# Optimization experiments

Hardware: AMD Instinct MI355X
Metric: run time of the kernel (lower is better)

The kernel has to match this reference:

```python
import jax, jax.numpy as jnp
import numpy as np
from jax import lax

B, T, N, F_IN, F_OUT, K = 16, 12, 2048, 32, 64, 3
TK = 3  # temporal kernel


def setup_inputs() -> dict:
    key = jax.random.key(0)
    ks = jax.random.split(key, 10)
    s = lambda fan: 1.0 / np.sqrt(fan)
    return {
        "x": jax.random.normal(ks[0], (B, T, N, F_IN), jnp.float32),
        "cheb": jax.random.normal(ks[1], (K, N, N), jnp.float32) * s(N),
        "wq_t": jax.random.normal(ks[2], (F_IN, 1), jnp.float32) * s(F_IN),
        "wk_t": jax.random.normal(ks[3], (F_IN, 1), jnp.float32) * s(F_IN),
        "wq_s": jax.random.normal(ks[4], (F_IN, 1), jnp.float32) * s(F_IN),
        "wk_s": jax.random.normal(ks[5], (F_IN, 1), jnp.float32) * s(F_IN),
        "theta": jax.random.normal(ks[6], (K, F_IN, F_OUT), jnp.float32) * s(F_IN),
        "tconv_w": jax.random.normal(ks[7], (F_OUT, F_OUT, TK, 1), jnp.float32) * s(F_OUT * TK),
        "tconv_b": jnp.zeros((F_OUT,), jnp.float32),
        "rconv_w": jax.random.normal(ks[8], (F_OUT, F_IN), jnp.float32) * s(F_IN),
        "rconv_b": jnp.zeros((F_OUT,), jnp.float32),
        "ln_g": jnp.ones((F_OUT,), jnp.float32),
        "ln_b": jnp.zeros((F_OUT,), jnp.float32),
    }


def reference(x, cheb, wq_t, wk_t, wq_s, wk_s, theta, tconv_w, tconv_b,
              rconv_w, rconv_b, ln_g, ln_b):
    b, t, n, f = x.shape
    # --- temporal attention: (B,T,T) over time, scaled by sqrt(N)
    qt = jnp.einsum('btnf,fo->btn', x, wq_t)  # (B,T,N)
    kt = jnp.einsum('btnf,fo->btn', x, wk_t)
    ta = jax.nn.softmax(jnp.einsum('btn,bsn->bts', qt, kt) / np.sqrt(n), axis=-1)
    x_ta = jnp.einsum('bts,bsnf->btnf', ta, x)
    # --- spatial attention: (B,N,N), scaled by sqrt(history_len)
    qs = jnp.einsum('btnf,fo->btn', x_ta, wq_s)
    ks_ = jnp.einsum('btnf,fo->btn', x_ta, wk_s)
    sa = jax.nn.softmax(jnp.einsum('btn,btm->bnm', qs, ks_) / np.sqrt(t), axis=-1)
    # --- Chebyshev graph conv with attention-weighted polynomials
    out = jnp.zeros((b, t, n, theta.shape[-1]), x.dtype)
    for kk in range(cheb.shape[0]):  # small fixed K
        tka = cheb[kk][None, :, :] * sa              # (B,N,N)
        rhs = jnp.einsum('bij,btjf->btif', tka, x_ta)  # (B,T,N,F_in)
        out = out + jnp.einsum('btif,fo->btio', rhs, theta[kk])
    x_gc = jax.nn.relu(out)  # (B,T,N,O)
    # --- temporal conv over T (kernel (3,1), pad (1,0)), NCHW with H=T, W=N
    xc = x_gc.transpose(0, 3, 1, 2)
    pad = TK // 2
    x_tc = lax.conv_general_dilated(
        xc, tconv_w, window_strides=(1, 1), padding=((pad, pad), (0, 0)),
        dimension_numbers=('NCHW', 'OIHW', 'NCHW'))
    x_tc = x_tc + tconv_b[None, :, None, None]
    # --- 1x1 residual conv on original x
    res = jnp.einsum('btnf,of->botn', x, rconv_w) + rconv_b[None, :, None, None]
    y = jax.nn.relu(x_tc + res).transpose(0, 2, 3, 1)  # (B,T,N,O)
    # --- layer norm over channels
    mu = jnp.mean(y, axis=-1, keepdims=True)
    var = jnp.mean((y - mu) ** 2, axis=-1, keepdims=True)
    return (y - mu) * lax.rsqrt(var + 1e-5) * ln_g + ln_b
```

## Files before the change

kernel.cpp:

```cpp
#include <hip/hip_runtime.h>
#include <hip/hip_bf16.h>
#include <math.h>

#define BB 16
#define TT 12
#define NN 2048
#define FIN 32
#define FOUT 64
#define KCH 3

typedef __attribute__((ext_vector_type(8))) short vbf16x8;
typedef __attribute__((ext_vector_type(4))) float vf32x4;

__device__ __forceinline__ float ldf(const void* p, size_t i, int mf) {
    if (mf) return ((const float*)p)[i];
    return __bfloat162float(((const __hip_bfloat16*)p)[i]);
}

__device__ __forceinline__ void load8d(const void* p, size_t i, int mf, float* o) {
    if (mf) {
        const float* fp = (const float*)p + i;
        float4 a = *(const float4*)fp;
        float4 b = *(const float4*)(fp + 4);
        o[0] = a.x; o[1] = a.y; o[2] = a.z; o[3] = a.w;
        o[4] = b.x; o[5] = b.y; o[6] = b.z; o[7] = b.w;
    } else {
        uint4 u = *(const uint4*)((const __hip_bfloat16*)p + i);
        const __hip_bfloat16* h = (const __hip_bfloat16*)&u;
#pragma unroll
        for (int j = 0; j < 8; ++j) o[j] = __bfloat162float(h[j]);
    }
}

__device__ __forceinline__ vbf16x8 pack8(const float* v) {
    union { vbf16x8 f; __hip_bfloat16 h[8]; } u;
#pragma unroll
    for (int j = 0; j < 8; ++j) u.h[j] = __float2bfloat16(v[j]);
    return u.f;
}

__global__ __launch_bounds__(256) void k_detect(const void* __restrict__ x, int* __restrict__ flag) {
    __shared__ int cnt[256];
    const unsigned short* h = (const unsigned short*)x;
    int bad = 0;
    for (int i = threadIdx.x; i < 4096; i += 256) {
        int e = (h[i] >> 7) & 0xFF;
        if (e < 110 || e > 133) bad++;
    }
    cnt[threadIdx.x] = bad;
    __syncthreads();
    for (int s = 128; s > 0; s >>= 1) {
        if ((int)threadIdx.x < s) cnt[threadIdx.x] += cnt[threadIdx.x + s];
        __syncthreads();
    }
    if (threadIdx.x == 0) flag[0] = (cnt[0] > 614) ? 1 : 0;
}

__global__ __launch_bounds__(256) void k_emergency(__hip_bfloat16* out, size_t n) {
    size_t i = (size_t)blockIdx.x * 256 + threadIdx.x;
    if (i < n) out[i] = __float2bfloat16(55555.f);
}

__global__ __launch_bounds__(256) void k_cvt_cheb(
    const void* __restrict__ cheb, const int* __restrict__ flag,
    __hip_bfloat16* __restrict__ chebBF) {
    int mf = flag[0];
    size_t i = ((size_t)blockIdx.x * 256 + threadIdx.x) * 8;
    float v[8];
    load8d(cheb, i, mf, v);
    union { uint4 u; __hip_bfloat16 h[8]; } pv;
#pragma unroll
    for (int j = 0; j < 8; ++j) pv.h[j] = __float2bfloat16(v[j]);
    *reinterpret_cast<uint4*>(&chebBF[i]) = pv.u;
}

__global__ __launch_bounds__(256) void k_prep(
    const void* __restrict__ theta, const void* __restrict__ tconv_w,
    const void* __restrict__ tconv_b, const void* __restrict__ rconv_w,
    const void* __restrict__ rconv_b, const int* __restrict__ flag,
    __hip_bfloat16* __restrict__ Tt, __hip_bfloat16* __restrict__ Wt, float* __restrict__ biasC) {
    int mf = flag[0];
    int tid = blockIdx.x * 256 + threadIdx.x;
    if (tid < 64 * 96) {
        int o = tid / 96, kf = tid % 96;
        Tt[tid] = __float2bfloat16(ldf(theta, (size_t)kf * 64 + o, mf));
    }
    if (tid < 64 * 224) {
        int o = tid / 224, c = tid % 224;
        float v;
        if (c < 192) {
            int dt = c / 64, i = c % 64;
            v = ldf(tconv_w, ((size_t)o * 64 + i) * 3 + dt, mf);
        } else {
            v = ldf(rconv_w, (size_t)o * 32 + (c - 192), mf);
        }
        Wt[tid] = __float2bfloat16(v);
    }
    if (tid < 64) biasC[tid] = ldf(tconv_b, tid, mf) + ldf(rconv_b, tid, mf);
}

__global__ __launch_bounds__(256) void k_qtkt(
    const void* __restrict__ x, const void* __restrict__ wq,
    const void* __restrict__ wk, const int* __restrict__ flag,
    float* __restrict__ qt, float* __restrict__ kt) {
    int mf = flag[0];
    __shared__ float swq[32], swk[32];
    if (threadIdx.x < 32) swq[threadIdx.x] = ldf(wq, threadIdx.x, mf);
    else if (threadIdx.x < 64) swk[threadIdx.x - 32] = ldf(wk, threadIdx.x - 32, mf);
    __syncthreads();
    size_t idx = (size_t)blockIdx.x * 256 + threadIdx.x;
    float q = 0.f, k = 0.f;
#pragma unroll
    for (int c = 0; c < 4; ++c) {
        float v[8];
        load8d(x, idx * FIN + c * 8, mf, v);
#pragma unroll
        for (int j = 0; j < 8; ++j) { q += v[j] * swq[c * 8 + j]; k += v[j] * swk[c * 8 + j]; }
    }
    qt[idx] = q;
    kt[idx] = k;
}

__global__ __launch_bounds__(256) void k_tattn(
    const float* __restrict__ qt, const float* __restrict__ kt, float* __restrict__ ta) {
    int b = blockIdx.x / TT, t = blockIdx.x % TT;
    const float* q = qt + ((size_t)b * TT + t) * NN;
    float part[TT];
#pragma unroll
    for (int s = 0; s < TT; ++s) part[s] = 0.f;
    for (int n = threadIdx.x; n < NN; n += 256) {
        float qv = q[n];
#pragma unroll
        for (int s = 0; s < TT; ++s) part[s] += qv * kt[((size_t)b * TT + s) * NN + n];
    }
    __shared__ float red[TT][4];
    __shared__ float sc[TT];
    int lane = threadIdx.x & 63, wid = threadIdx.x >> 6;
#pragma unroll
    for (int s = 0; s < TT; ++s) {
        float v = part[s];
#pragma unroll
        for (int m = 32; m >= 1; m >>= 1) v += __shfl_xor(v, m);
        if (lane == 0) red[s][wid] = v;
    }
    __syncthreads();
    if (threadIdx.x < TT)
        sc[threadIdx.x] = (red[threadIdx.x][0] + red[threadIdx.x][1] + red[threadIdx.x][2] +
                           red[threadIdx.x][3]) * 0.02209708691207961f;
    __syncthreads();
    if (threadIdx.x == 0) {
        float m = sc[0];
#pragma unroll
        for (int s = 1; s < TT; ++s) m = fmaxf(m, sc[s]);
        float e[TT], sum = 0.f;
#pragma unroll
        for (int s = 0; s < TT; ++s) { e[s] = __expf(sc[s] - m); sum += e[s]; }
        float inv = 1.f / sum;
#pragma unroll
        for (int s = 0; s < TT; ++s) ta[((size_t)b * TT + t) * TT + s] = e[s] * inv;
    }
}

__global__ __launch_bounds__(256) void k_xta(
    const void* __restrict__ x, const float* __restrict__ ta,
    const void* __restrict__ wqs, const void* __restrict__ wks, const int* __restrict__ flag,
    __hip_bfloat16* __restrict__ xT, float* __restrict__ qs, float* __restrict__ ks, int b0) {
    int mf = flag[0];
    int gid = blockIdx.x * 256 + threadIdx.x;
    int fg = gid & 3;
    int n = (gid >> 2) & (NN - 1);
    int bl = gid >> 13;
    int b = b0 + bl;
    __shared__ float sta[TT * TT];
    __shared__ float swq[32], swk[32];
    if (threadIdx.x < 144) sta[threadIdx.x] = ta[(size_t)b * 144 + threadIdx.x];
    else if (threadIdx.x >= 160 && threadIdx.x < 192) swq[threadIdx.x - 160] = ldf(wqs, threadIdx.x - 160, mf);
    else if (threadIdx.x >= 192 && threadIdx.x < 224) swk[threadIdx.x - 192] = ldf(wks, threadIdx.x - 192, mf);
    __syncthreads();

    float acc[TT][8];
#pragma unroll
    for (int t = 0; t < TT; ++t)
#pragma unroll
        for (int j = 0; j < 8; ++j) acc[t][j] = 0.f;

    for (int s = 0; s < TT; ++s) {
        float xv[8];
        load8d(x, (((size_t)(b * TT + s) * NN) + n) * FIN + fg * 8, mf, xv);
#pragma unroll
        for (int t = 0; t < TT; ++t) {
            float w = sta[t * TT + s];
#pragma unroll
            for (int j = 0; j < 8; ++j) acc[t][j] += w * xv[j];
        }
    }
    size_t xbase = (size_t)bl * 384 * NN;
#pragma unroll
    for (int t = 0; t < TT; ++t)
#pragma unroll
        for (int j = 0; j < 8; ++j)
            xT[xbase + (size_t)(t * 32 + fg * 8 + j) * NN + n] = __float2bfloat16(acc[t][j]);
#pragma unroll
    for (int t = 0; t < TT; ++t) {
        float pq = 0.f, pk = 0.f;
#pragma unroll
        for (int j = 0; j < 8; ++j) {
            pq += acc[t][j] * swq[fg * 8 + j];
            pk += acc[t][j] * swk[fg * 8 + j];
        }
        pq += __shfl_xor(pq, 1); pq += __shfl_xor(pq, 2);
        pk += __shfl_xor(pk, 1); pk += __shfl_xor(pk, 2);
        if (fg == 0) {
            qs[((size_t)b * NN + n) * TT + t] = pq;
            ks[((size_t)b * NN + n) * TT + t] = pk;
        }
    }
}

__global__ __launch_bounds__(256) void k_sattn(
    const float* __restrict__ qs, const float* __restrict__ ks,
    __hip_bfloat16* __restrict__ sa, int b0) {
    int bl = blockIdx.x >> 8;
    int b = b0 + bl;
    int i0 = (blockIdx.x & 255) * 8;
    __shared__ float qrow[8][TT];
    __shared__ float rbuf[4];
    if (threadIdx.x < 96) qrow[threadIdx.x / TT][threadIdx.x % TT] =
        qs[((size_t)b * NN + i0) * TT + threadIdx.x];
    __syncthreads();
    const float scale = 0.28867513459481287f;
    float sc[8][8];
#pragma unroll
    for (int c = 0; c < 8; ++c) {
        int j = threadIdx.x + (c << 8);
        const float* kr = ks + ((size_t)b * NN + j) * TT;
        float kv[TT];
        *(float4*)&kv[0] = *(const float4*)&kr[0];
        *(float4*)&kv[4] = *(const float4*)&kr[4];
        *(float4*)&kv[8] = *(const float4*)&kr[8];
#pragma unroll
        for (int r = 0; r < 8; ++r) {
            float d = 0.f;
#pragma unroll
            for (int t = 0; t < TT; ++t) d += qrow[r][t] * kv[t];
            sc[r][c] = d * scale;
        }
    }
    int lane = threadIdx.x & 63, wid = threadIdx.x >> 6;
#pragma unroll
    for (int r = 0; r < 8; ++r) {
        float v = -1e30f;
#pragma unroll
        for (int c = 0; c < 8; ++c) v = fmaxf(v, sc[r][c]);
#pragma unroll
        for (int m = 32; m >= 1; m >>= 1) v = fmaxf(v, __shfl_xor(v, m));
        if (lane == 0) rbuf[wid] = v;
        __syncthreads();
        float bmax = fmaxf(fmaxf(rbuf[0], rbuf[1]), fmaxf(rbuf[2], rbuf[3]));
        __syncthreads();
        float lsum = 0.f;
#pragma unroll
        for (int c = 0; c < 8; ++c) { float e = __expf(sc[r][c] - bmax); sc[r][c] = e; lsum += e; }
        v = lsum;
#pragma unroll
        for (int m = 32; m >= 1; m >>= 1) v += __shfl_xor(v, m);
        if (lane == 0) rbuf[wid] = v;
        __syncthreads();
        float inv = 1.f / (rbuf[0] + rbuf[1] + rbuf[2] + rbuf[3]);
        __syncthreads();
        size_t base = ((size_t)bl * NN + i0 + r) * NN + threadIdx.x;
#pragma unroll
        for (int c = 0; c < 8; ++c) sa[base + (c << 8)] = __float2bfloat16(sc[r][c] * inv);
    }
}

__global__ __launch_bounds__(256, 2) void k_gemm_cheb(
    const __hip_bfloat16* __restrict__ chebBF, const __hip_bfloat16* __restrict__ sa,
    const __hip_bfloat16* __restrict__ xT, __hip_bfloat16* __restrict__ rhs) {
    int it = blockIdx.x;
    int bz = blockIdx.y;
    int bl = bz / 3, kk = bz % 3;

    __shared__ __hip_bfloat16 As[2][64][40];

    int tid = threadIdx.x;
    int wid = tid >> 6, lane = tid & 63;
    int wn = wid * 96;
    int lr = lane & 15, kq = (lane >> 4) * 8;

    const size_t i0 = (size_t)it * 64;
    const __hip_bfloat16* chebK = chebBF + (size_t)kk * NN * NN;
    const __hip_bfloat16* saB = sa + (size_t)bl * NN * NN;
    const __hip_bfloat16* xTB = xT + (size_t)bl * 384 * NN;

    int srow = tid >> 2;
    int scol = (tid & 3) * 8;

    const __hip_bfloat16* cptr = &chebK[(i0 + srow) * NN + scol];
    const __hip_bfloat16* sptr = &saB[(i0 + srow) * NN + scol];
    const __hip_bfloat16* bptr0 = &xTB[(size_t)(wn + lr) * NN + kq];

    vf32x4 acc[4][6];
    vf32x4 z4 = {0.f, 0.f, 0.f, 0.f};
#pragma unroll
    for (int mi = 0; mi < 4; ++mi)
#pragma unroll
        for (int ni = 0; ni < 6; ++ni) acc[mi][ni] = z4;

    uint4 cu = *reinterpret_cast<const uint4*>(cptr);
    uint4 su = *reinterpret_cast<const uint4*>(sptr);
    vbf16x8 bcur[6];
#pragma unroll
    for (int ni = 0; ni < 6; ++ni)
        bcur[ni] = *reinterpret_cast<const vbf16x8*>(bptr0 + (size_t)(ni * 16) * NN);

    for (int step = 0; step < 64; ++step) {
        int p = step & 1;
        {
            const __hip_bfloat16* ch = (const __hip_bfloat16*)&cu;
            const __hip_bfloat16* sh = (const __hip_bfloat16*)&su;
            union { uint4 u; __hip_bfloat16 h8[8]; } pv;
#pragma unroll
            for (int j = 0; j < 8; ++j)
                pv.h8[j] = __float2bfloat16(__bfloat162float(ch[j]) * __bfloat162float(sh[j]));
            *reinterpret_cast<uint4*>(&As[p][srow][scol]) = pv.u;
        }

        __syncthreads();

        vbf16x8 a[4];
#pragma unroll
        for (int mi = 0; mi < 4; ++mi)
            a[mi] = *reinterpret_cast<const vbf16x8*>(&As[p][mi * 16 + lr][kq]);

        int joff = (step < 63) ? (step + 1) * 32 : step * 32;
        cu = *reinterpret_cast<const uint4*>(cptr + joff);
        su = *reinterpret_cast<const uint4*>(sptr + joff);
        vbf16x8 bnxt[6];
#pragma unroll
        for (int ni = 0; ni < 6; ++ni)
            bnxt[ni] = *reinterpret_cast<const vbf16x8*>(bptr0 + (size_t)(ni * 16) * NN + joff);

#pragma unroll
        for (int ni = 0; ni < 6; ++ni)
#pragma unroll
            for (int mi = 0; mi < 4; ++mi)
                acc[mi][ni] = __builtin_amdgcn_mfma_f32_16x16x32_bf16(a[mi], bcur[ni], acc[mi][ni], 0, 0, 0);

#pragma unroll
        for (int ni = 0; ni < 6; ++ni) bcur[ni] = bnxt[ni];
    }
#pragma unroll
    for (int mi = 0; mi < 4; ++mi)
#pragma unroll
        for (int ni = 0; ni < 6; ++ni)
#pragma unroll
            for (int g = 0; g < 4; ++g) {
                int row = mi * 16 + ((lane >> 4) << 2) + g;
                int col = wn + ni * 16 + lr;
                size_t i = i0 + row;
                int t = col >> 5, f = col & 31;
                rhs[(((size_t)bl * NN + i) * TT + t) * 96 + kk * 32 + f] =
                    __float2bfloat16(acc[mi][ni][g]);
            }
}

__global__ __launch_bounds__(256) void k_theta(
    const __hip_bfloat16* __restrict__ rhs, const __hip_bfloat16* __restrict__ Tt,
    __hip_bfloat16* __restrict__ G) {
    __shared__ __hip_bfloat16 Ts[64][104];
    int tid = threadIdx.x;
    int srow = tid >> 2, scol = (tid & 3) * 8;
#pragma unroll
    for (int c0 = 0; c0 < 96; c0 += 32)
        *reinterpret_cast<uint4*>(&Ts[srow][c0 + scol]) =
            *reinterpret_cast<const uint4*>(&Tt[(size_t)srow * 96 + c0 + scol]);
    __syncthreads();
    int wid = tid >> 6, lane = tid & 63;
    int lr = lane & 15, kq = (lane >> 4) * 8;
    size_t r0 = (size_t)blockIdx.x * 128 + wid * 32;
    vf32x4 acc[2][4];
    vf32x4 z4 = {0.f, 0.f, 0.f, 0.f};
#pragma unroll
    for (int mi = 0; mi < 2; ++mi)
#pragma unroll
        for (int ni = 0; ni < 4; ++ni) acc[mi][ni] = z4;
#pragma unroll
    for (int s = 0; s < 3; ++s) {
        vbf16x8 a[2], bf[4];
#pragma unroll
        for (int mi = 0; mi < 2; ++mi)
            a[mi] = *reinterpret_cast<const vbf16x8*>(&rhs[(r0 + mi * 16 + lr) * 96 + s * 32 + kq]);
#pragma unroll
        for (int ni = 0; ni < 4; ++ni)
            bf[ni] = *reinterpret_cast<const vbf16x8*>(&Ts[ni * 16 + lr][s * 32 + kq]);
#pragma unroll
        for (int mi = 0; mi < 2; ++mi)
#pragma unroll
            for (int ni = 0; ni < 4; ++ni)
                acc[mi][ni] = __builtin_amdgcn_mfma_f32_16x16x32_bf16(a[mi], bf[ni], acc[mi][ni], 0, 0, 0);
    }
#pragma unroll
    for (int mi = 0; mi < 2; ++mi)
#pragma unroll
        for (int ni = 0; ni < 4; ++ni)
#pragma unroll
            for (int g = 0; g < 4; ++g) {
                size_t r = r0 + mi * 16 + ((lane >> 4) << 2) + g;
                int col = ni * 16 + (lane & 15);
                int t = (int)(r % TT);
                size_t bn = r / TT;
                int n = (int)(bn & (NN - 1));
                int bl = (int)(bn >> 11);
                float v = fmaxf(acc[mi][ni][g], 0.f);
                G[(((size_t)bl * TT + t) * NN + n) * 64 + col] = __float2bfloat16(v);
            }
}

__global__ __launch_bounds__(256) void k_final(
    const __hip_bfloat16* __restrict__ G, const void* __restrict__ x,
    const __hip_bfloat16* __restrict__ Wt, const float* __restrict__ biasC,
    const void* __restrict__ ln_g, const void* __restrict__ ln_b,
    const int* __restrict__ flag, void* __restrict__ outv, int b0) {
    int mf = flag[0];
    int n0 = blockIdx.x * 128;
    int t = blockIdx.y;
    int bl = blockIdx.z;
    int b = b0 + bl;
    __shared__ __hip_bfloat16 Ws[64][232];
    __shared__ float sg[64], sb[64], sbias[64];
    int tid = threadIdx.x;
    int srow = tid >> 2, scol = (tid & 3) * 8;
#pragma unroll
    for (int c0 = 0; c0 < 224; c0 += 32)
        *reinterpret_cast<uint4*>(&Ws[srow][c0 + scol]) =
            *reinterpret_cast<const uint4*>(&Wt[(size_t)srow * 224 + c0 + scol]);
    if (tid < 64) {
        sg[tid] = ldf(ln_g, tid, mf);
        sb[tid] = ldf(ln_b, tid, mf);
        sbias[tid] = biasC[tid];
    }
    __syncthreads();
    int wid = tid >> 6, lane = tid & 63;
    int lr = lane & 15, kq = (lane >> 4) * 8;
    int rw = n0 + wid * 32;
    vf32x4 acc[2][4];
    vf32x4 z4 = {0.f, 0.f, 0.f, 0.f};
#pragma unroll
    for (int mi = 0; mi < 2; ++mi)
#pragma unroll
        for (int ni = 0; ni < 4; ++ni) acc[mi][ni] = z4;

    vbf16x8 zfrag = {0, 0, 0, 0, 0, 0, 0, 0};
#pragma unroll
    for (int s = 0; s < 7; ++s) {
        int kb = s * 32;
        vbf16x8 a[2], bf[4];
#pragma unroll
        for (int ni = 0; ni < 4; ++ni)
            bf[ni] = *reinterpret_cast<const vbf16x8*>(&Ws[ni * 16 + lr][kb + kq]);
        if (s < 6) {
            int dt = s >> 1;
            int t2 = t + dt - 1;
            int off = (s & 1) * 32 + kq;
            if (t2 >= 0 && t2 < TT) {
#pragma unroll
                for (int mi = 0; mi < 2; ++mi)
                    a[mi] = *reinterpret_cast<const vbf16x8*>(
                        &G[(((size_t)bl * TT + t2) * NN + rw + mi * 16 + lr) * 64 + off]);
            } else {
                a[0] = zfrag; a[1] = zfrag;
            }
        } else {
#pragma unroll
            for (int mi = 0; mi < 2; ++mi) {
                float xv[8];
                load8d(x, (((size_t)b * TT + t) * NN + rw + mi * 16 + lr) * FIN + kq, mf, xv);
                a[mi] = pack8(xv);
            }
        }
#pragma unroll
        for (int mi = 0; mi < 2; ++mi)
#pragma unroll
            for (int ni = 0; ni < 4; ++ni)
                acc[mi][ni] = __builtin_amdgcn_mfma_f32_16x16x32_bf16(a[mi], bf[ni], acc[mi][ni], 0, 0, 0);
    }
    float vals[2][4][4];
#pragma unroll
    for (int mi = 0; mi < 2; ++mi)
#pragma unroll
        for (int ni = 0; ni < 4; ++ni) {
            int col = ni * 16 + lr;
#pragma unroll
            for (int g = 0; g < 4; ++g)
                vals[mi][ni][g] = fmaxf(acc[mi][ni][g] + sbias[col], 0.f);
        }
#pragma unroll
    for (int mi = 0; mi < 2; ++mi)
#pragma unroll
        for (int g = 0; g < 4; ++g) {
            float s1 = 0.f, s2 = 0.f;
#pragma unroll
            for (int ni = 0; ni < 4; ++ni) { float v = vals[mi][ni][g]; s1 += v; s2 += v * v; }
            s1 += __shfl_xor(s1, 1); s2 += __shfl_xor(s2, 1);
            s1 += __shfl_xor(s1, 2); s2 += __shfl_xor(s2, 2);
            s1 += __shfl_xor(s1, 4); s2 += __shfl_xor(s2, 4);
            s1 += __shfl_xor(s1, 8); s2 += __shfl_xor(s2, 8);
            float mean = s1 * (1.f / 64.f);
            float var = fmaxf(s2 * (1.f / 64.f) - mean * mean, 0.f);
            float rstd = rsqrtf(var + 1e-5f);
            int row = wid * 32 + mi * 16 + ((lane >> 4) << 2) + g;
#pragma unroll
            for (int ni = 0; ni < 4; ++ni) {
                int col = ni * 16 + lr;
                float y = (vals[mi][ni][g] - mean) * rstd * sg[col] + sb[col];
                size_t oi = (((size_t)b * TT + t) * NN + n0 + row) * 64 + col;
                if (mf) ((float*)outv)[oi] = y;
                else ((__hip_bfloat16*)outv)[oi] = __float2bfloat16(y);
            }
        }
}

extern "C" void kernel_launch(void* const* d_in, const int* in_sizes, int n_in,
                              void* d_out, int out_size, void* d_ws, size_t ws_size,
                              hipStream_t stream) {
    const void* x      = d_in[0];
    const void* cheb   = d_in[1];
    const void* wq_t   = d_in[2];
    const void* wk_t   = d_in[3];
    const void* wq_s   = d_in[4];
    const void* wk_s   = d_in[5];
    const void* theta  = d_in[6];
    const void* tconvw = d_in[7];
    const void* tconvb = d_in[8];
    const void* rconvw = d_in[9];
    const void* rconvb = d_in[10];
    const void* ln_g   = d_in[11];
    const void* ln_b   = d_in[12];

    const size_t sflag = 256;
    const size_t sqt   = (size_t)BB * TT * NN * 4;
    const size_t sta   = 16384;
    const size_t sTt   = 64 * 96 * 2;
    const size_t sWt   = 64 * 224 * 2;
    const size_t sbias = 256;
    const size_t scheb = (size_t)KCH * NN * NN * 2;
    const size_t fixed = sflag + 2 * sqt + sta + sTt + sWt + sbias + scheb;
    const size_t pxT  = (size_t)384 * NN * 2;
    const size_t psa  = (size_t)NN * NN * 2;
    const size_t prhs = (size_t)NN * TT * 96 * 2;
    const size_t perb = pxT + psa + prhs;

    int chk = 0;
    for (int c = 16; c >= 1; c >>= 1)
        if (fixed + (size_t)c * perb <= ws_size) { chk = c; break; }

    if (chk == 0) {
        k_emergency<<<(out_size + 255) / 256, 256, 0, stream>>>(
            (__hip_bfloat16*)d_out, (size_t)out_size);
        return;
    }

    char* ws = (char*)d_ws;
    size_t off = 0;
    int*   flag = (int*)(ws + off);             off += sflag;
    float* qt   = (float*)(ws + off);           off += sqt;
    float* kt   = (float*)(ws + off);           off += sqt;
    float* ta   = (float*)(ws + off);           off += sta;
    __hip_bfloat16* Tt = (__hip_bfloat16*)(ws + off);  off += sTt;
    __hip_bfloat16* Wt = (__hip_bfloat16*)(ws + off);  off += sWt;
    float* biasC = (float*)(ws + off);          off += sbias;
    __hip_bfloat16* chebBF = (__hip_bfloat16*)(ws + off); off += scheb;
    __hip_bfloat16* xTc  = (__hip_bfloat16*)(ws + off); off += (size_t)chk * pxT;
    __hip_bfloat16* saC  = (__hip_bfloat16*)(ws + off); off += (size_t)chk * psa;
    __hip_bfloat16* rhsC = (__hip_bfloat16*)(ws + off); off += (size_t)chk * prhs;
    float* qs = qt;
    float* ks = kt;
    __hip_bfloat16* Gc = saC;

    k_detect<<<1, 256, 0, stream>>>(x, flag);
    k_cvt_cheb<<<(KCH * NN * NN) / 2048, 256, 0, stream>>>(cheb, flag, chebBF);
    k_prep<<<56, 256, 0, stream>>>(theta, tconvw, tconvb, rconvw, rconvb, flag, Tt, Wt, biasC);
    k_qtkt<<<(BB * TT * NN) / 256, 256, 0, stream>>>(x, wq_t, wk_t, flag, qt, kt);
    k_tattn<<<BB * TT, 256, 0, stream>>>(qt, kt, ta);
    for (int b0 = 0; b0 < BB; b0 += chk) {
        k_xta<<<(chk * NN * 4) / 256, 256, 0, stream>>>(x, ta, wq_s, wk_s, flag, xTc, qs, ks, b0);
        k_sattn<<<chk * (NN / 8), 256, 0, stream>>>(qs, ks, saC, b0);
        k_gemm_cheb<<<dim3(32, chk * KCH), 256, 0, stream>>>(chebBF, saC, xTc, rhsC);
        k_theta<<<(chk * NN * TT) / 128, 256, 0, stream>>>(rhsC, Tt, Gc);
        k_final<<<dim3(NN / 128, TT, chk), 256, 0, stream>>>(Gc, x, Wt, biasC, ln_g, ln_b, flag, d_out, b0);
    }
}
```

Measured before the change: 691.2 us.

## Drop LDS staging in cheb GEMM, load A fragments directly with register double-buffering

The Chebyshev-attention GEMM no longer builds the cheb*sa product in shared memory behind a per-step barrier. Each wave now loads its own A fragments from global memory, multiplies them in registers, and double-buffers both A and B loads across two k-steps. The M tile shrinks from 64 to 32 rows and the grid doubles to match. This removes __syncthreads and the LDS round trip. In exchange, every wave re-reads the same A rows (four times the cheb/sa global traffic per block) and B is reused over fewer rows, so more xT traffic overall.

```diff
diff --git a/kernel.cpp b/kernel.cpp
--- a/kernel.cpp
+++ b/kernel.cpp
@@ -36,6 +36,16 @@
     union { vbf16x8 f; __hip_bfloat16 h[8]; } u;
 #pragma unroll
     for (int j = 0; j < 8; ++j) u.h[j] = __float2bfloat16(v[j]);
+    return u.f;
+}
+
+__device__ __forceinline__ vbf16x8 mulpack8(uint4 c, uint4 s) {
+    const __hip_bfloat16* ch = (const __hip_bfloat16*)&c;
+    const __hip_bfloat16* sh = (const __hip_bfloat16*)&s;
+    union { vbf16x8 f; __hip_bfloat16 h[8]; } u;
+#pragma unroll
+    for (int j = 0; j < 8; ++j)
+        u.h[j] = __float2bfloat16(__bfloat162float(ch[j]) * __bfloat162float(sh[j]));
     return u.f;
 }
 
@@ -281,77 +291,64 @@
     int bz = blockIdx.y;
     int bl = bz / 3, kk = bz % 3;
 
-    __shared__ __hip_bfloat16 As[2][64][40];
-
     int tid = threadIdx.x;
     int wid = tid >> 6, lane = tid & 63;
     int wn = wid * 96;
     int lr = lane & 15, kq = (lane >> 4) * 8;
 
-    const size_t i0 = (size_t)it * 64;
-    const __hip_bfloat16* chebK = chebBF + (size_t)kk * NN * NN;
-    const __hip_bfloat16* saB = sa + (size_t)bl * NN * NN;
-    const __hip_bfloat16* xTB = xT + (size_t)bl * 384 * NN;
-
-    int srow = tid >> 2;
-    int scol = (tid & 3) * 8;
-
-    const __hip_bfloat16* cptr = &chebK[(i0 + srow) * NN + scol];
-    const __hip_bfloat16* sptr = &saB[(i0 + srow) * NN + scol];
-    const __hip_bfloat16* bptr0 = &xTB[(size_t)(wn + lr) * NN + kq];
-
-    vf32x4 acc[4][6];
+    const size_t i0 = (size_t)it * 32;
+    const __hip_bfloat16* cA = chebBF + (size_t)kk * NN * NN + (i0 + lr) * NN + kq;
+    const __hip_bfloat16* sA = sa + (size_t)bl * NN * NN + (i0 + lr) * NN + kq;
+    const __hip_bfloat16* bp = xT + (size_t)bl * 384 * NN + (size_t)(wn + lr) * NN + kq;
+
+    vf32x4 acc[2][6];
     vf32x4 z4 = {0.f, 0.f, 0.f, 0.f};
 #pragma unroll
-    for (int mi = 0; mi < 4; ++mi)
+    for (int mi = 0; mi < 2; ++mi)
 #pragma unroll
         for (int ni = 0; ni < 6; ++ni) acc[mi][ni] = z4;
 
-    uint4 cu = *reinterpret_cast<const uint4*>(cptr);
-    uint4 su = *reinterpret_cast<const uint4*>(sptr);
-    vbf16x8 bcur[6];
-#pragma unroll
-    for (int ni = 0; ni < 6; ++ni)
-        bcur[ni] = *reinterpret_cast<const vbf16x8*>(bptr0 + (size_t)(ni * 16) * NN);
-
-    for (int step = 0; step < 64; ++step) {
-        int p = step & 1;
-        {
-            const __hip_bfloat16* ch = (const __hip_bfloat16*)&cu;
-            const __hip_bfloat16* sh = (const __hip_bfloat16*)&su;
-            union { uint4 u; __hip_bfloat16 h8[8]; } pv;
-#pragma unroll
-            for (int j = 0; j < 8; ++j)
-                pv.h8[j] = __float2bfloat16(__bfloat162float(ch[j]) * __bfloat162float(sh[j]));
-            *reinterpret_cast<uint4*>(&As[p][srow][scol]) = pv.u;
-        }
-
-        __syncthreads();
-
-        vbf16x8 a[4];
-#pragma unroll
-        for (int mi = 0; mi < 4; ++mi)
-            a[mi] = *reinterpret_cast<const vbf16x8*>(&As[p][mi * 16 + lr][kq]);
-
-        int joff = (step < 63) ? (step + 1) * 32 : step * 32;
-        cu = *reinterpret_cast<const uint4*>(cptr + joff);
-        su = *reinterpret_cast<const uint4*>(sptr + joff);
-        vbf16x8 bnxt[6];
-#pragma unroll
-        for (int ni = 0; ni < 6; ++ni)
-            bnxt[ni] = *reinterpret_cast<const vbf16x8*>(bptr0 + (size_t)(ni * 16) * NN + joff);
-
-#pragma unroll
-        for (int ni = 0; ni < 6; ++ni)
-#pragma unroll
-            for (int mi = 0; mi < 4; ++mi)
-                acc[mi][ni] = __builtin_amdgcn_mfma_f32_16x16x32_bf16(a[mi], bcur[ni], acc[mi][ni], 0, 0, 0);
-
-#pragma unroll
-        for (int ni = 0; ni < 6; ++ni) bcur[ni] = bnxt[ni];
-    }
-#pragma unroll
-    for (int mi = 0; mi < 4; ++mi)
+    uint4 cu0[2], su0[2], cu1[2], su1[2];
+    vbf16x8 b0[6], b1[6];
+
+#define K6_LOAD(CU, SU, BV, J)                                                      \
+    {                                                                               \
+        size_t jo = (size_t)(J) * 32;                                               \
+        CU[0] = *reinterpret_cast<const uint4*>(cA + jo);                           \
+        CU[1] = *reinterpret_cast<const uint4*>(cA + (size_t)16 * NN + jo);         \
+        SU[0] = *reinterpret_cast<const uint4*>(sA + jo);                           \
+        SU[1] = *reinterpret_cast<const uint4*>(sA + (size_t)16 * NN + jo);         \
+        _Pragma("unroll")                                                           \
+        for (int ni = 0; ni < 6; ++ni)                                              \
+            BV[ni] = *reinterpret_cast<const vbf16x8*>(bp + (size_t)(ni * 16) * NN + jo); \
+    }
+
+#define K6_COMP(CU, SU, BV)                                                         \
+    {                                                                               \
+        vbf16x8 afr[2];                                                             \
+        _Pragma("unroll")                                                           \
+        for (int mi = 0; mi < 2; ++mi) afr[mi] = mulpack8(CU[mi], SU[mi]);          \
+        _Pragma("unroll")                                                           \
+        for (int ni = 0; ni < 6; ++ni)                                              \
+            _Pragma("unroll")                                                       \
+            for (int mi = 0; mi < 2; ++mi)                                          \
+                acc[mi][ni] = __builtin_amdgcn_mfma_f32_16x16x32_bf16(              \
+                    afr[mi], BV[ni], acc[mi][ni], 0, 0, 0);                         \
+    }
+
+    K6_LOAD(cu0, su0, b0, 0);
+    for (int step = 0; step < 64; step += 2) {
+        K6_LOAD(cu1, su1, b1, step + 1);
+        K6_COMP(cu0, su0, b0);
+        int j2 = (step + 2 < 64) ? step + 2 : 63;
+        K6_LOAD(cu0, su0, b0, j2);
+        K6_COMP(cu1, su1, b1);
+    }
+#undef K6_LOAD
+#undef K6_COMP
+
+#pragma unroll
+    for (int mi = 0; mi < 2; ++mi)
 #pragma unroll
         for (int ni = 0; ni < 6; ++ni)
 #pragma unroll
@@ -586,7 +583,7 @@
     for (int b0 = 0; b0 < BB; b0 += chk) {
         k_xta<<<(chk * NN * 4) / 256, 256, 0, stream>>>(x, ta, wq_s, wk_s, flag, xTc, qs, ks, b0);
         k_sattn<<<chk * (NN / 8), 256, 0, stream>>>(qs, ks, saC, b0);
-        k_gemm_cheb<<<dim3(32, chk * KCH), 256, 0, stream>>>(chebBF, saC, xTc, rhsC);
+        k_gemm_cheb<<<dim3(64, chk * KCH), 256, 0, stream>>>(chebBF, saC, xTc, rhsC);
         k_theta<<<(chk * NN * TT) / 128, 256, 0, stream>>>(rhsC, Tt, Gc);
         k_final<<<dim3(NN / 128, TT, chk), 256, 0, stream>>>(Gc, x, Wt, biasC, ln_g, ln_b, flag, d_out, b0);
     }
```

Measured after the change: 1.487 ms. 115% more time.

## Stage Chebyshev GEMM B operand through LDS via async global_load_lds

Applied to the files above, without the earlier changes.

The B operand (xT) of the Chebyshev GEMM is now loaded with direct global-to-LDS async loads into a double-buffered, XOR-swizzled shared buffer, rather than held in per-lane registers. Each step reads B fragments from LDS while prefetching the next tile. The grid is also reordered so the three Chebyshev orders for the same row tile run as adjacent blocks, which should improve L2 reuse of the attention rows. This is meant to cut register pressure and global load latency, at the cost of about 49 KB of extra LDS per block, which may reduce occupancy. Correctness relies on the compiler inserting the right vmcnt waits for the LDS DMA.

```diff
diff --git a/kernel.cpp b/kernel.cpp
--- a/kernel.cpp
+++ b/kernel.cpp
@@ -37,6 +37,22 @@
 #pragma unroll
     for (int j = 0; j < 8; ++j) u.h[j] = __float2bfloat16(v[j]);
     return u.f;
+}
+
+__device__ __forceinline__ uint4 mulpack8u(uint4 c, uint4 s) {
+    const __hip_bfloat16* ch = (const __hip_bfloat16*)&c;
+    const __hip_bfloat16* sh = (const __hip_bfloat16*)&s;
+    union { uint4 u; __hip_bfloat16 h[8]; } o;
+#pragma unroll
+    for (int j = 0; j < 8; ++j)
+        o.h[j] = __float2bfloat16(__bfloat162float(ch[j]) * __bfloat162float(sh[j]));
+    return o.u;
+}
+
+__device__ __forceinline__ void gload16(const __hip_bfloat16* g, __hip_bfloat16* l) {
+    __builtin_amdgcn_global_load_lds(
+        (const __attribute__((address_space(1))) unsigned int*)g,
+        (__attribute__((address_space(3))) unsigned int*)l, 16, 0, 0);
 }
 
 __global__ __launch_bounds__(256) void k_detect(const void* __restrict__ x, int* __restrict__ flag) {
@@ -277,11 +293,11 @@
 __global__ __launch_bounds__(256, 2) void k_gemm_cheb(
     const __hip_bfloat16* __restrict__ chebBF, const __hip_bfloat16* __restrict__ sa,
     const __hip_bfloat16* __restrict__ xT, __hip_bfloat16* __restrict__ rhs) {
-    int it = blockIdx.x;
-    int bz = blockIdx.y;
-    int bl = bz / 3, kk = bz % 3;
+    int it = blockIdx.x / 3, kk = blockIdx.x % 3;
+    int bl = blockIdx.y;
 
     __shared__ __hip_bfloat16 As[2][64][40];
+    __shared__ __hip_bfloat16 Bs[2][384 * 32];
 
     int tid = threadIdx.x;
     int wid = tid >> 6, lane = tid & 63;
@@ -295,10 +311,12 @@
 
     int srow = tid >> 2;
     int scol = (tid & 3) * 8;
-
     const __hip_bfloat16* cptr = &chebK[(i0 + srow) * NN + scol];
     const __hip_bfloat16* sptr = &saB[(i0 + srow) * NN + scol];
-    const __hip_bfloat16* bptr0 = &xTB[(size_t)(wn + lr) * NN + kq];
+
+    int brow = wn + (lane >> 2);
+    int gck = ((lane & 3) ^ ((lane >> 2) & 3)) * 8;
+    const __hip_bfloat16* bsrc = &xTB[(size_t)brow * NN + gck];
 
     vf32x4 acc[4][6];
     vf32x4 z4 = {0.f, 0.f, 0.f, 0.f};
@@ -309,47 +327,44 @@
 
     uint4 cu = *reinterpret_cast<const uint4*>(cptr);
     uint4 su = *reinterpret_cast<const uint4*>(sptr);
-    vbf16x8 bcur[6];
-#pragma unroll
-    for (int ni = 0; ni < 6; ++ni)
-        bcur[ni] = *reinterpret_cast<const vbf16x8*>(bptr0 + (size_t)(ni * 16) * NN);
+#pragma unroll
+    for (int v = 0; v < 6; ++v)
+        gload16(bsrc + (size_t)(v * 16) * NN, &Bs[0][(wn + v * 16) * 32]);
 
     for (int step = 0; step < 64; ++step) {
         int p = step & 1;
         {
-            const __hip_bfloat16* ch = (const __hip_bfloat16*)&cu;
-            const __hip_bfloat16* sh = (const __hip_bfloat16*)&su;
-            union { uint4 u; __hip_bfloat16 h8[8]; } pv;
-#pragma unroll
-            for (int j = 0; j < 8; ++j)
-                pv.h8[j] = __float2bfloat16(__bfloat162float(ch[j]) * __bfloat162float(sh[j]));
-            *reinterpret_cast<uint4*>(&As[p][srow][scol]) = pv.u;
-        }
-
+            uint4 pv = mulpack8u(cu, su);
+            *reinterpret_cast<uint4*>(&As[p][srow][scol]) = pv;
+        }
         __syncthreads();
 
         vbf16x8 a[4];
 #pragma unroll
         for (int mi = 0; mi < 4; ++mi)
             a[mi] = *reinterpret_cast<const vbf16x8*>(&As[p][mi * 16 + lr][kq]);
-
-        int joff = (step < 63) ? (step + 1) * 32 : step * 32;
-        cu = *reinterpret_cast<const uint4*>(cptr + joff);
-        su = *reinterpret_cast<const uint4*>(sptr + joff);
-        vbf16x8 bnxt[6];
+        vbf16x8 b[6];
+#pragma unroll
+        for (int ni = 0; ni < 6; ++ni) {
+            int r = wn + ni * 16 + lr;
+            int pos = ((kq >> 3) ^ (r & 3)) * 8;
+            b[ni] = *reinterpret_cast<const vbf16x8*>(&Bs[p][r * 32 + pos]);
+        }
+
+        int k0n = (step < 63) ? (step + 1) * 32 : step * 32;
+        cu = *reinterpret_cast<const uint4*>(cptr + k0n);
+        su = *reinterpret_cast<const uint4*>(sptr + k0n);
+#pragma unroll
+        for (int v = 0; v < 6; ++v)
+            gload16(bsrc + (size_t)(v * 16) * NN + k0n, &Bs[p ^ 1][(wn + v * 16) * 32]);
+
 #pragma unroll
         for (int ni = 0; ni < 6; ++ni)
-            bnxt[ni] = *reinterpret_cast<const vbf16x8*>(bptr0 + (size_t)(ni * 16) * NN + joff);
-
-#pragma unroll
-        for (int ni = 0; ni < 6; ++ni)
 #pragma unroll
             for (int mi = 0; mi < 4; ++mi)
-                acc[mi][ni] = __builtin_amdgcn_mfma_f32_16x16x32_bf16(a[mi], bcur[ni], acc[mi][ni], 0, 0, 0);
-
-#pragma unroll
-        for (int ni = 0; ni < 6; ++ni) bcur[ni] = bnxt[ni];
-    }
+                acc[mi][ni] = __builtin_amdgcn_mfma_f32_16x16x32_bf16(a[mi], b[ni], acc[mi][ni], 0, 0, 0);
+    }
+
 #pragma unroll
     for (int mi = 0; mi < 4; ++mi)
 #pragma unroll
@@ -586,7 +601,7 @@
     for (int b0 = 0; b0 < BB; b0 += chk) {
         k_xta<<<(chk * NN * 4) / 256, 256, 0, stream>>>(x, ta, wq_s, wk_s, flag, xTc, qs, ks, b0);
         k_sattn<<<chk * (NN / 8), 256, 0, stream>>>(qs, ks, saC, b0);
-        k_gemm_cheb<<<dim3(32, chk * KCH), 256, 0, stream>>>(chebBF, saC, xTc, rhsC);
+        k_gemm_cheb<<<dim3(96, chk), 256, 0, stream>>>(chebBF, saC, xTc, rhsC);
         k_theta<<<(chk * NN * TT) / 128, 256, 0, stream>>>(rhsC, Tt, Gc);
         k_final<<<dim3(NN / 128, TT, chk), 256, 0, stream>>>(Gc, x, Wt, biasC, ln_g, ln_b, flag, d_out, b0);
     }
```

After: 630.1 us. 8.8% less time.
